# Performance work log

Hardware: AMD Instinct MI355X
Metric: run time of the kernel (lower is better)

The kernel has to match this reference:

```python
import jax, jax.numpy as jnp
import numpy as np

B, S, D, H, V, N_SHARDS, CAP = 4, 512, 512, 8, 32000, 64, 128
HD = D // H


def _layernorm(x, g, b, eps=1e-5):
    mu = x.mean(-1, keepdims=True)
    var = ((x - mu) ** 2).mean(-1, keepdims=True)
    return (x - mu) * jax.lax.rsqrt(var + eps) * g + b


def setup_inputs() -> dict:
    key = jax.random.key(0)
    ks = jax.random.split(key, 16)
    s = 0.02
    return {
        'input_ids': jax.random.randint(ks[0], (B, S), 0, V, dtype=jnp.int32),
        'emb': jax.random.normal(ks[1], (V, D), jnp.float32) * s,
        'Wq': jax.random.normal(ks[2], (D, D), jnp.float32) * s,
        'Wk': jax.random.normal(ks[3], (D, D), jnp.float32) * s,
        'Wv': jax.random.normal(ks[4], (D, D), jnp.float32) * s,
        'Wo': jax.random.normal(ks[5], (D, D), jnp.float32) * s,
        'ln_g': jnp.ones((D,), jnp.float32),
        'ln_b': jnp.zeros((D,), jnp.float32),
        'W_router': jax.random.normal(ks[6], (D, N_SHARDS), jnp.float32),
        'mem_keys': jax.random.normal(ks[7], (N_SHARDS, CAP, D), jnp.float32) * s,
        'mem_values': jax.random.normal(ks[8], (N_SHARDS, CAP, D), jnp.float32) * s,
        'Wg_c': jax.random.normal(ks[9], (D, D), jnp.float32) * s,
        'Wg_m': jax.random.normal(ks[10], (D, D), jnp.float32) * s,
        'bg': jnp.zeros((D,), jnp.float32),
        'Wd': jax.random.normal(ks[11], (D, V), jnp.float32) * s,
        'bd': jnp.zeros((V,), jnp.float32),
        'top_k': 4,
    }


def reference(input_ids, emb, Wq, Wk, Wv, Wo, ln_g, ln_b, W_router,
              mem_keys, mem_values, Wg_c, Wg_m, bg, Wd, bd, top_k):
    # --- encode_context: embedding + causal MHA block (ContextSynthesizer) ---
    x = emb[input_ids]                                   # [B,S,D]
    q = (x @ Wq).reshape(B, S, H, HD)
    k = (x @ Wk).reshape(B, S, H, HD)
    v = (x @ Wv).reshape(B, S, H, HD)
    att = jnp.einsum('bqhd,bkhd->bhqk', q, k) / jnp.sqrt(jnp.float32(HD))
    causal = jnp.tril(jnp.ones((S, S), bool))
    att = jnp.where(causal[None, None], att, jnp.finfo(att.dtype).min)
    att = jax.nn.softmax(att, axis=-1)
    o = jnp.einsum('bhqk,bkhd->bqhd', att, v).reshape(B, S, D) @ Wo
    ctx = _layernorm(x + o, ln_g, ln_b)                  # [B,S,D]

    # --- LSHRouter: hyperplane projection -> shard id per token ---
    routes = jnp.argmax(ctx @ W_router, axis=-1)         # [B,S] int

    # --- MemoryShardStore.query, batched: per-token routed shard top-k read ---
    keys_g = mem_keys[routes]                            # [B,S,CAP,D] irregular gather
    scores = jnp.einsum('bscd,bsd->bsc', keys_g, ctx)    # [B,S,CAP]
    top_v, top_i = jax.lax.top_k(scores, top_k)          # [B,S,k]
    w = jax.nn.softmax(top_v, axis=-1)
    vals = mem_values[routes[:, :, None], top_i]         # [B,S,k,D]
    memory_stream = jnp.einsum('bsk,bskd->bsd', w, vals)

    # --- GatedMemoryFusion ---
    gate = jax.nn.sigmoid(ctx @ Wg_c + memory_stream @ Wg_m + bg)
    fused = gate * ctx + (1.0 - gate) * memory_stream

    # --- decoder; payload bias is zero (store holds no sequence_chunk records) ---
    logits = fused @ Wd + bd                             # [B,S,V]
    return logits
```

## Files before the change

### kernel.cpp

```cpp
#include <hip/hip_runtime.h>

typedef unsigned short u16;
typedef float f32x4 __attribute__((ext_vector_type(4)));
typedef short short8 __attribute__((ext_vector_type(8)));
typedef __bf16 bf16x8 __attribute__((ext_vector_type(8)));

#define B_  4
#define S_  512
#define D_  512
#define H_  8
#define HD_ 64
#define V_  32000
#define NSHARD_ 64
#define CAP_ 128
#define TOK_ (B_ * S_)

__device__ __forceinline__ float bf2f(u16 u) { return __uint_as_float(((unsigned)u) << 16); }
__device__ __forceinline__ u16 f2bf(float f) {
  unsigned u = __float_as_uint(f);
  u += 0x7FFFu + ((u >> 16) & 1u);
  return (u16)(u >> 16);
}

__device__ __forceinline__ f32x4 mfma16(short8 a, short8 b, f32x4 c) {
  return __builtin_amdgcn_mfma_f32_16x16x32_bf16(
      __builtin_bit_cast(bf16x8, a), __builtin_bit_cast(bf16x8, b), c, 0, 0, 0);
}

__device__ __forceinline__ void load_lds16(const void* g, void* l) {
  __builtin_amdgcn_global_load_lds(
      (const __attribute__((address_space(1))) void*)g,
      (__attribute__((address_space(3))) void*)l, 16, 0, 0);
}

template<int NS, bool ACC, int OM, bool CSKIP, bool CKLIM>
__global__ __launch_bounds__(256) void gemm_bt(
    const u16* __restrict__ Ah, const u16* __restrict__ Al, int ldA, long sA1, long sA2,
    const u16* __restrict__ Bh, const u16* __restrict__ Bl, int ldB, long sB1, long sB2,
    void* __restrict__ C0, void* __restrict__ C1, int ldC, long sC1, long sC2,
    int K, int z2n, float alpha)
{
  __shared__ u16 AsH[64 * 64];
  __shared__ u16 BsH[64 * 64];
  __shared__ u16 AsL[(NS == 3) ? 64 * 64 : 8];
  __shared__ u16 BsL[(NS == 3) ? 64 * 64 : 8];

  const int n0 = blockIdx.x * 64;
  const int m0 = blockIdx.y * 64;
  if (CSKIP && n0 > m0 + 63) return;

  const int z = blockIdx.z;
  const int z1 = z / z2n, z2 = z - z1 * z2n;
  const long baseA = (long)z1 * sA1 + (long)z2 * sA2;
  const long baseB = (long)z1 * sB1 + (long)z2 * sB2;
  const long baseC = (long)z1 * sC1 + (long)z2 * sC2;

  const int tid = threadIdx.x;
  const int lane = tid & 63;
  const int w = tid >> 6;
  const int wm = (w >> 1) * 32, wn = (w & 1) * 32;
  const int fr = lane & 15, kg = lane >> 4;

  const int srow = lane >> 3;
  const int schunk = (lane & 7) ^ srow;

  const u16* gAh = Ah + baseA + (long)(m0 + w * 16 + srow) * ldA + schunk * 8;
  const u16* gBh = Bh + baseB + (long)(n0 + w * 16 + srow) * ldB + schunk * 8;
  const u16* gAl = (NS == 3) ? (Al + baseA + (long)(m0 + w * 16 + srow) * ldA + schunk * 8) : nullptr;
  const u16* gBl = (NS == 3) ? (Bl + baseB + (long)(n0 + w * 16 + srow) * ldB + schunk * 8) : nullptr;
  u16* lAh = &AsH[(w * 16) * 64];
  u16* lBh = &BsH[(w * 16) * 64];
  u16* lAl = &AsL[(NS == 3) ? (w * 16) * 64 : 0];
  u16* lBl = &BsL[(NS == 3) ? (w * 16) * 64 : 0];

  const int kmax = CKLIM ? (m0 + 64) : K;

  f32x4 acc[2][2] = {};

  for (int k0 = 0; k0 < kmax; k0 += 64) {
    load_lds16(gAh + k0, lAh);
    load_lds16(gAh + k0 + 8 * ldA, lAh + 8 * 64);
    load_lds16(gBh + k0, lBh);
    load_lds16(gBh + k0 + 8 * ldB, lBh + 8 * 64);
    if (NS == 3) {
      load_lds16(gAl + k0, lAl);
      load_lds16(gAl + k0 + 8 * ldA, lAl + 8 * 64);
      load_lds16(gBl + k0, lBl);
      load_lds16(gBl + k0 + 8 * ldB, lBl + 8 * 64);
    }
    __syncthreads();

    short8 ah[2][2], bh[2][2], al[2][2], bl[2][2];
#pragma unroll
    for (int mi = 0; mi < 2; ++mi) {
      int row = wm + mi * 16 + fr;
#pragma unroll
      for (int ks = 0; ks < 2; ++ks) {
        int idx = row * 64 + ((ks * 32 + kg * 8) ^ ((fr & 7) << 3));
        ah[mi][ks] = *(const short8*)&AsH[idx];
        if (NS == 3) al[mi][ks] = *(const short8*)&AsL[idx];
      }
    }
#pragma unroll
    for (int ni = 0; ni < 2; ++ni) {
      int row = wn + ni * 16 + fr;
#pragma unroll
      for (int ks = 0; ks < 2; ++ks) {
        int idx = row * 64 + ((ks * 32 + kg * 8) ^ ((fr & 7) << 3));
        bh[ni][ks] = *(const short8*)&BsH[idx];
        if (NS == 3) bl[ni][ks] = *(const short8*)&BsL[idx];
      }
    }
#pragma unroll
    for (int ks = 0; ks < 2; ++ks)
#pragma unroll
      for (int mi = 0; mi < 2; ++mi)
#pragma unroll
        for (int ni = 0; ni < 2; ++ni) {
          acc[mi][ni] = mfma16(ah[mi][ks], bh[ni][ks], acc[mi][ni]);
          if (NS == 3) {
            acc[mi][ni] = mfma16(ah[mi][ks], bl[ni][ks], acc[mi][ni]);
            acc[mi][ni] = mfma16(al[mi][ks], bh[ni][ks], acc[mi][ni]);
          }
        }
    __syncthreads();
  }

#pragma unroll
  for (int mi = 0; mi < 2; ++mi)
#pragma unroll
    for (int ni = 0; ni < 2; ++ni) {
      int gnc = n0 + wn + ni * 16 + fr;
#pragma unroll
      for (int r = 0; r < 4; ++r) {
        int gm = m0 + wm + mi * 16 + kg * 4 + r;
        float v = acc[mi][ni][r] * alpha;
        long idx = baseC + (long)gm * ldC + gnc;
        if (OM == 0) {
          float* C = (float*)C0;
          C[idx] = ACC ? (C[idx] + v) : v;
        } else {
          u16 h = f2bf(v);
          ((u16*)C0)[idx] = h;
          ((u16*)C1)[idx] = f2bf(v - bf2f(h));
        }
      }
    }
}

__global__ __launch_bounds__(256) void logits_gemm_k(
    const u16* __restrict__ A, const u16* __restrict__ Bt,
    const float* __restrict__ bias, float* __restrict__ C)
{
  __shared__ u16 As[128 * 64];
  __shared__ u16 Bs[128 * 64];
  const int id = blockIdx.x * 16 + blockIdx.y;
  const int swz = (id & 7) * 500 + (id >> 3);
  const int n0 = (swz / 16) * 128;
  const int m0 = (swz % 16) * 128;
  const int tid = threadIdx.x;
  const int lane = tid & 63;
  const int w = tid >> 6;
  const int wm = (w >> 1) * 64, wn = (w & 1) * 64;
  const int fr = lane & 15, kg = lane >> 4;

  const int srow = lane >> 3;
  const int schunk = (lane & 7) ^ srow;
  const u16* gA = A + (long)(m0 + w * 32 + srow) * D_ + schunk * 8;
  const u16* gB = Bt + (long)(n0 + w * 32 + srow) * D_ + schunk * 8;
  u16* lA = &As[(w * 32) * 64];
  u16* lB = &Bs[(w * 32) * 64];

  f32x4 acc[4][4] = {};

  for (int kt = 0; kt < D_; kt += 64) {
#pragma unroll
    for (int i = 0; i < 4; ++i) {
      load_lds16(gA + (long)i * 8 * D_ + kt, lA + i * 8 * 64);
      load_lds16(gB + (long)i * 8 * D_ + kt, lB + i * 8 * 64);
    }
    __syncthreads();

    short8 af[4][2], bf[4][2];
#pragma unroll
    for (int mi = 0; mi < 4; ++mi) {
      int row = wm + mi * 16 + fr;
#pragma unroll
      for (int ks = 0; ks < 2; ++ks)
        af[mi][ks] = *(const short8*)&As[row * 64 +
                         ((ks * 32 + kg * 8) ^ ((fr & 7) << 3))];
    }
#pragma unroll
    for (int ni = 0; ni < 4; ++ni) {
      int row = wn + ni * 16 + fr;
#pragma unroll
      for (int ks = 0; ks < 2; ++ks)
        bf[ni][ks] = *(const short8*)&Bs[row * 64 +
                         ((ks * 32 + kg * 8) ^ ((fr & 7) << 3))];
    }
#pragma unroll
    for (int ks = 0; ks < 2; ++ks)
#pragma unroll
      for (int mi = 0; mi < 4; ++mi)
#pragma unroll
        for (int ni = 0; ni < 4; ++ni)
          acc[mi][ni] = mfma16(af[mi][ks], bf[ni][ks], acc[mi][ni]);
    __syncthreads();
  }

#pragma unroll
  for (int ni = 0; ni < 4; ++ni) {
    int gnc = n0 + wn + ni * 16 + fr;
    float bv = bias[gnc];
#pragma unroll
    for (int mi = 0; mi < 4; ++mi)
#pragma unroll
      for (int r = 0; r < 4; ++r) {
        int gm = m0 + wm + mi * 16 + kg * 4 + r;
        C[(long)gm * V_ + gnc] = acc[mi][ni][r] + bv;
      }
  }
}

template<bool LO>
__global__ __launch_bounds__(256) void transpose_split_k(
    const float* __restrict__ W, int ldw,
    u16* __restrict__ oh, u16* __restrict__ ol)
{
  __shared__ float t[64][65];
  const int n0 = blockIdx.x * 64;
  const int k0 = blockIdx.y * 64;
  const int tid = threadIdx.x;
  {
    const int kk = tid >> 4;
    const int c4 = (tid & 15) * 4;
#pragma unroll
    for (int i = 0; i < 4; ++i) {
      f32x4 v = *(const f32x4*)(W + (long)(k0 + kk + i * 16) * ldw + n0 + c4);
      t[kk + i * 16][c4] = v[0];
      t[kk + i * 16][c4 + 1] = v[1];
      t[kk + i * 16][c4 + 2] = v[2];
      t[kk + i * 16][c4 + 3] = v[3];
    }
  }
  __syncthreads();
  {
    const int chunk = tid & 7;
    const int nn = tid >> 3;
#pragma unroll
    for (int j = 0; j < 2; ++j) {
      int n = nn + j * 32;
      u16 hbuf[8], lbuf[8];
#pragma unroll
      for (int e = 0; e < 8; ++e) {
        float fv = t[chunk * 8 + e][n];
        u16 h = f2bf(fv);
        hbuf[e] = h;
        if (LO) lbuf[e] = f2bf(fv - bf2f(h));
      }
      long ob = (long)(n0 + n) * 512 + k0 + chunk * 8;
      *(short8*)(oh + ob) = *(short8*)hbuf;
      if (LO) *(short8*)(ol + ob) = *(short8*)lbuf;
    }
  }
}

__global__ __launch_bounds__(256) void v_transpose_k(
    const u16* __restrict__ qh, const u16* __restrict__ ql,
    u16* __restrict__ vTh, u16* __restrict__ vTl)
{
  __shared__ u16 th[64][68];
  __shared__ u16 tl[64][68];
  const int z = blockIdx.y;
  const int b = z >> 3, h = z & 7;
  const int s0 = blockIdx.x * 64;
  const long ibase = ((long)(b * 512 + s0)) * 1536 + 1024 + h * 64;
  const int tid = threadIdx.x;
  {
    const int sr = tid >> 2;
    const int c8 = (tid & 3) * 16;
    const long src = ibase + (long)sr * 1536 + c8;
    *(short8*)&th[sr][c8]     = *(const short8*)(qh + src);
    *(short8*)&th[sr][c8 + 8] = *(const short8*)(qh + src + 8);
    *(short8*)&tl[sr][c8]     = *(const short8*)(ql + src);
    *(short8*)&tl[sr][c8 + 8] = *(const short8*)(ql + src + 8);
  }
  __syncthreads();
  {
    const int dr = tid >> 2;
    const int s8 = (tid & 3) * 16;
    u16 oh[16], ol[16];
#pragma unroll
    for (int j = 0; j < 16; ++j) { oh[j] = th[s8 + j][dr]; ol[j] = tl[s8 + j][dr]; }
    long ob = (long)z * 64 * 512 + (long)dr * 512 + s0 + s8;
    *(short8*)(vTh + ob)     = *(short8*)&oh[0];
    *(short8*)(vTh + ob + 8) = *(short8*)&oh[8];
    *(short8*)(vTl + ob)     = *(short8*)&ol[0];
    *(short8*)(vTl + ob + 8) = *(short8*)&ol[8];
  }
}

__global__ __launch_bounds__(128) void embed_k(const int* __restrict__ ids,
                                               const float* __restrict__ emb,
                                               float* __restrict__ x,
                                               u16* __restrict__ xh,
                                               u16* __restrict__ xl) {
  const int t = blockIdx.x;
  const long id = ids[t];
  const int c = threadIdx.x * 4;
  f32x4 v = *(const f32x4*)(emb + id * (long)D_ + c);
  *(f32x4*)(x + (long)t * D_ + c) = v;
  u16 hh[4], ll[4];
#pragma unroll
  for (int j = 0; j < 4; ++j) {
    u16 h = f2bf(v[j]);
    hh[j] = h;
    ll[j] = f2bf(v[j] - bf2f(h));
  }
  *(unsigned long long*)(xh + (long)t * D_ + c) = *(unsigned long long*)hh;
  *(unsigned long long*)(xl + (long)t * D_ + c) = *(unsigned long long*)ll;
}

__global__ __launch_bounds__(64) void softmax_causal_k(
    const float* __restrict__ att, u16* __restrict__ ph, u16* __restrict__ pl) {
  const int row = blockIdx.x;
  const int i = row & 511;
  const float* p = att + ((long)row << 9);
  const int lane = threadIdx.x;
  float vals[8];
  float m = -3.4e38f;
#pragma unroll
  for (int it = 0; it < 8; ++it) {
    vals[it] = -3.4e38f;
    if (it * 64 <= i) {
      int j = it * 64 + lane;
      float v = (j <= i) ? p[j] : -3.4e38f;
      vals[it] = v;
      m = fmaxf(m, v);
    }
  }
#pragma unroll
  for (int off = 32; off; off >>= 1) m = fmaxf(m, __shfl_xor(m, off));
  float s = 0.f;
#pragma unroll
  for (int it = 0; it < 8; ++it) {
    if (it * 64 <= i) {
      int j = it * 64 + lane;
      float e = (j <= i) ? expf(vals[it] - m) : 0.f;
      vals[it] = e;
      s += e;
    }
  }
#pragma unroll
  for (int off = 32; off; off >>= 1) s += __shfl_xor(s, off);
  float inv = 1.f / s;
#pragma unroll
  for (int it = 0; it < 8; ++it) {
    if (it * 64 <= i) {
      long ob = ((long)row << 9) + it * 64 + lane;
      float e = vals[it] * inv;
      u16 h = f2bf(e);
      ph[ob] = h;
      pl[ob] = f2bf(e - bf2f(h));
    }
  }
}

__global__ __launch_bounds__(256) void resid_ln_k(
    const float* __restrict__ x, const float* __restrict__ proj,
    const float* __restrict__ g, const float* __restrict__ b,
    float* __restrict__ ctxf, u16* __restrict__ ctxh)
{
  const int t = blockIdx.x;
  const int tid = threadIdx.x;
  __shared__ float red[8];
  const float* xr = x + (long)t * D_;
  const float* pr = proj + (long)t * D_;
  float v0 = xr[tid] + pr[tid];
  float v1 = xr[tid + 256] + pr[tid + 256];
  float s = v0 + v1, q = v0 * v0 + v1 * v1;
#pragma unroll
  for (int off = 32; off; off >>= 1) { s += __shfl_xor(s, off); q += __shfl_xor(q, off); }
  const int wave = tid >> 6, lane = tid & 63;
  if (lane == 0) { red[wave] = s; red[4 + wave] = q; }
  __syncthreads();
  s = red[0] + red[1] + red[2] + red[3];
  q = red[4] + red[5] + red[6] + red[7];
  float mu = s * (1.f / 512.f);
  float var = q * (1.f / 512.f) - mu * mu;
  float rs = rsqrtf(var + 1e-5f);
  float o0 = (v0 - mu) * rs * g[tid] + b[tid];
  float o1 = (v1 - mu) * rs * g[tid + 256] + b[tid + 256];
  long base = (long)t * D_;
  ctxf[base + tid] = o0;
  ctxf[base + tid + 256] = o1;
  ctxh[base + tid] = f2bf(o0);
  ctxh[base + tid + 256] = f2bf(o1);
}

__global__ __launch_bounds__(128) void route_mem_k(
    const float* __restrict__ ctxf, const float* __restrict__ Wr,
    const float* __restrict__ keys, const float* __restrict__ valsm,
    float* __restrict__ msf, u16* __restrict__ msh)
{
  const int t = blockIdx.x;
  const int tid = threadIdx.x;
  __shared__ float sctx[D_];
  __shared__ float spart[CAP_];
  __shared__ float sred2[2][64];
  __shared__ int s_route;
  __shared__ int sidx[4];
  __shared__ float sw[4];

  f32x4 cv = ((const f32x4*)(ctxf + (long)t * D_))[tid];
  ((f32x4*)sctx)[tid] = cv;
  __syncthreads();

  {
    const int c = tid & 63, half = tid >> 6;
    float accr = 0.f;
    const float* cp = sctx + half * 256;
    const float* wp = Wr + (long)(half * 256) * NSHARD_ + c;
    for (int d = 0; d < 256; ++d) accr += cp[d] * wp[(long)d * NSHARD_];
    sred2[half][c] = accr;
  }
  __syncthreads();
  if (tid < 64) {
    float v = sred2[0][tid] + sred2[1][tid];
    int idx = tid;
#pragma unroll
    for (int off = 32; off; off >>= 1) {
      float ov = __shfl_xor(v, off);
      int oi = __shfl_xor(idx, off);
      if (ov > v || (ov == v && oi < idx)) { v = ov; idx = oi; }
    }
    if (tid == 0) s_route = idx;
  }
  __syncthreads();
  const int route = s_route;

  {
    const float* krow = keys + ((long)route * CAP_ + tid) * D_;
    float sc = 0.f;
    for (int d0 = 0; d0 < D_; d0 += 4) {
      f32x4 kv = *(const f32x4*)(krow + d0);
      sc += sctx[d0] * kv[0] + sctx[d0 + 1] * kv[1] +
            sctx[d0 + 2] * kv[2] + sctx[d0 + 3] * kv[3];
    }
    spart[tid] = sc;
  }
  __syncthreads();

  for (int rep = 0; rep < 4; ++rep) {
    if (tid < 64) {
      float v1 = spart[tid]; int i1 = tid;
      float v2 = spart[tid + 64]; int i2 = tid + 64;
      float v; int idx;
      if (v2 > v1) { v = v2; idx = i2; } else { v = v1; idx = i1; }
#pragma unroll
      for (int off = 32; off; off >>= 1) {
        float ov = __shfl_xor(v, off);
        int oi = __shfl_xor(idx, off);
        if (ov > v || (ov == v && oi < idx)) { v = ov; idx = oi; }
      }
      if (tid == 0) { sidx[rep] = idx; sw[rep] = v; spart[idx] = -3.4e38f; }
    }
    __syncthreads();
  }

  float w0 = sw[0], w1 = sw[1], w2 = sw[2], w3 = sw[3];
  float mx = fmaxf(fmaxf(w0, w1), fmaxf(w2, w3));
  float e0 = expf(w0 - mx), e1 = expf(w1 - mx), e2 = expf(w2 - mx), e3 = expf(w3 - mx);
  float inv = 1.f / (e0 + e1 + e2 + e3);
  float wk[4] = {e0 * inv, e1 * inv, e2 * inv, e3 * inv};

  float a0 = 0, a1 = 0, a2 = 0, a3 = 0;
#pragma unroll
  for (int k = 0; k < 4; ++k) {
    const float* vr = valsm + ((long)route * CAP_ + sidx[k]) * D_ + tid * 4;
    f32x4 vv = *(const f32x4*)vr;
    float w = wk[k];
    a0 += w * vv[0]; a1 += w * vv[1]; a2 += w * vv[2]; a3 += w * vv[3];
  }
  long ob = (long)t * D_ + tid * 4;
  f32x4 of; of[0] = a0; of[1] = a1; of[2] = a2; of[3] = a3;
  *(f32x4*)(msf + ob) = of;
  u16 oh[4];
  oh[0] = f2bf(a0); oh[1] = f2bf(a1); oh[2] = f2bf(a2); oh[3] = f2bf(a3);
  *(unsigned long long*)(msh + ob) = *(unsigned long long*)oh;
}

__global__ __launch_bounds__(256) void gate_fuse_k(
    const float* __restrict__ g1, const float* __restrict__ bg,
    const float* __restrict__ ctxf, const float* __restrict__ msf,
    u16* __restrict__ fused)
{
  long base = ((long)blockIdx.x * 256 + threadIdx.x) * 4;
  f32x4 gv = *(const f32x4*)(g1 + base);
  f32x4 cv = *(const f32x4*)(ctxf + base);
  f32x4 mv = *(const f32x4*)(msf + base);
  int col = (int)(base & 511);
  u16 o[4];
#pragma unroll
  for (int j = 0; j < 4; ++j) {
    float g = 1.f / (1.f + expf(-(gv[j] + bg[col + j])));
    o[j] = f2bf(g * cv[j] + (1.f - g) * mv[j]);
  }
  *(unsigned long long*)(fused + base) = *(unsigned long long*)o;
}

extern "C" void kernel_launch(void* const* d_in, const int* in_sizes, int n_in,
                              void* d_out, int out_size, void* d_ws, size_t ws_size,
                              hipStream_t stream) {
  const int*   ids  = (const int*)d_in[0];
  const float* emb  = (const float*)d_in[1];
  const float* Wq   = (const float*)d_in[2];
  const float* Wk   = (const float*)d_in[3];
  const float* Wv   = (const float*)d_in[4];
  const float* Wo   = (const float*)d_in[5];
  const float* ln_g = (const float*)d_in[6];
  const float* ln_b = (const float*)d_in[7];
  const float* Wr   = (const float*)d_in[8];
  const float* mk   = (const float*)d_in[9];
  const float* mv   = (const float*)d_in[10];
  const float* Wgc  = (const float*)d_in[11];
  const float* Wgm  = (const float*)d_in[12];
  const float* bg   = (const float*)d_in[13];
  const float* Wd   = (const float*)d_in[14];
  const float* bd   = (const float*)d_in[15];
  float* out = (float*)d_out;

  char* ws = (char*)d_ws;
  size_t off = 0;
  auto alloc = [&](size_t bytes) -> void* {
    void* p = ws + off;
    off += (bytes + 255) & ~(size_t)255;
    return p;
  };
  float* x      = (float*)alloc((size_t)TOK_ * D_ * 4);
  u16*   xh     = (u16*)  alloc((size_t)TOK_ * D_ * 2);
  u16*   xl     = (u16*)  alloc((size_t)TOK_ * D_ * 2);
  u16*   wqkvTh = (u16*)  alloc((size_t)3 * D_ * D_ * 2);
  u16*   wqkvTl = (u16*)  alloc((size_t)3 * D_ * D_ * 2);
  u16*   woTh   = (u16*)  alloc((size_t)D_ * D_ * 2);
  u16*   woTl   = (u16*)  alloc((size_t)D_ * D_ * 2);
  u16*   wgcTh  = (u16*)  alloc((size_t)D_ * D_ * 2);
  u16*   wgmTh  = (u16*)  alloc((size_t)D_ * D_ * 2);
  u16*   wdT    = (u16*)  alloc((size_t)D_ * V_ * 2);
  u16*   qkvh   = (u16*)  alloc((size_t)TOK_ * 3 * D_ * 2);
  u16*   qkvl   = (u16*)  alloc((size_t)TOK_ * 3 * D_ * 2);
  u16*   vTh    = (u16*)  alloc((size_t)B_ * H_ * HD_ * S_ * 2);
  u16*   vTl    = (u16*)  alloc((size_t)B_ * H_ * HD_ * S_ * 2);
  float* att    = (float*)alloc((size_t)B_ * H_ * S_ * S_ * 4);
  u16*   ph     = (u16*)  alloc((size_t)B_ * H_ * S_ * S_ * 2);
  u16*   pl     = (u16*)  alloc((size_t)B_ * H_ * S_ * S_ * 2);
  u16*   oh     = (u16*)  alloc((size_t)TOK_ * D_ * 2);
  u16*   ol     = (u16*)  alloc((size_t)TOK_ * D_ * 2);
  float* proj   = (float*)alloc((size_t)TOK_ * D_ * 4);
  float* ctxf   = (float*)alloc((size_t)TOK_ * D_ * 4);
  u16*   ctxh   = (u16*)  alloc((size_t)TOK_ * D_ * 2);
  float* msf    = (float*)alloc((size_t)TOK_ * D_ * 4);
  u16*   msh    = (u16*)  alloc((size_t)TOK_ * D_ * 2);
  float* g1     = (float*)alloc((size_t)TOK_ * D_ * 4);
  u16*   fused  = (u16*)  alloc((size_t)TOK_ * D_ * 2);

  {
    dim3 g8(D_ / 64, D_ / 64, 1);
    transpose_split_k<true><<<g8, 256, 0, stream>>>(Wq, D_, wqkvTh, wqkvTl);
    transpose_split_k<true><<<g8, 256, 0, stream>>>(Wk, D_, wqkvTh + D_ * D_, wqkvTl + D_ * D_);
    transpose_split_k<true><<<g8, 256, 0, stream>>>(Wv, D_, wqkvTh + 2 * D_ * D_, wqkvTl + 2 * D_ * D_);
    transpose_split_k<true><<<g8, 256, 0, stream>>>(Wo, D_, woTh, woTl);
    transpose_split_k<false><<<g8, 256, 0, stream>>>(Wgc, D_, wgcTh, nullptr);
    transpose_split_k<false><<<g8, 256, 0, stream>>>(Wgm, D_, wgmTh, nullptr);
    dim3 gd(V_ / 64, D_ / 64, 1);
    transpose_split_k<false><<<gd, 256, 0, stream>>>(Wd, V_, wdT, nullptr);
  }

  embed_k<<<TOK_, 128, 0, stream>>>(ids, emb, x, xh, xl);

  {
    dim3 g(1536 / 64, TOK_ / 64, 1);
    gemm_bt<3, false, 1, false, false><<<g, 256, 0, stream>>>(
        xh, xl, D_, 0, 0, wqkvTh, wqkvTl, D_, 0, 0,
        qkvh, qkvl, 1536, 0, 0, D_, 1, 1.f);
  }

  {
    dim3 g(S_ / 64, B_ * H_, 1);
    v_transpose_k<<<g, 256, 0, stream>>>(qkvh, qkvl, vTh, vTl);
  }

  {
    dim3 g(S_ / 64, S_ / 64, B_ * H_);
    gemm_bt<3, false, 0, true, false><<<g, 256, 0, stream>>>(
        qkvh, qkvl, 1536, (long)S_ * 1536, 64,
        qkvh + D_, qkvl + D_, 1536, (long)S_ * 1536, 64,
        att, nullptr, S_, (long)H_ * S_ * S_, (long)S_ * S_,
        HD_, H_, 0.125f);
  }

  softmax_causal_k<<<B_ * H_ * S_, 64, 0, stream>>>(att, ph, pl);

  {
    dim3 g(1, S_ / 64, B_ * H_);
    gemm_bt<3, false, 1, false, true><<<g, 256, 0, stream>>>(
        ph, pl, S_, (long)H_ * S_ * S_, (long)S_ * S_,
        vTh, vTl, S_, (long)H_ * HD_ * S_, (long)HD_ * S_,
        oh, ol, D_, (long)S_ * D_, HD_,
        S_, H_, 1.f);
  }

  {
    dim3 g(D_ / 64, TOK_ / 64, 1);
    gemm_bt<3, false, 0, false, false><<<g, 256, 0, stream>>>(
        oh, ol, D_, 0, 0, woTh, woTl, D_, 0, 0,
        proj, nullptr, D_, 0, 0, D_, 1, 1.f);
  }

  resid_ln_k<<<TOK_, 256, 0, stream>>>(x, proj, ln_g, ln_b, ctxf, ctxh);

  route_mem_k<<<TOK_, 128, 0, stream>>>(ctxf, Wr, mk, mv, msf, msh);

  {
    dim3 g(D_ / 64, TOK_ / 64, 1);
    gemm_bt<1, false, 0, false, false><<<g, 256, 0, stream>>>(
        ctxh, nullptr, D_, 0, 0, wgcTh, nullptr, D_, 0, 0,
        g1, nullptr, D_, 0, 0, D_, 1, 1.f);
    gemm_bt<1, true, 0, false, false><<<g, 256, 0, stream>>>(
        msh, nullptr, D_, 0, 0, wgmTh, nullptr, D_, 0, 0,
        g1, nullptr, D_, 0, 0, D_, 1, 1.f);
  }

  gate_fuse_k<<<(TOK_ * D_) / (256 * 4), 256, 0, stream>>>(g1, bg, ctxf, msf, fused);

  {
    dim3 g(V_ / 128, TOK_ / 128, 1);
    logits_gemm_k<<<g, 256, 0, stream>>>(fused, wdT, bd, out);
  }
}
```

Measured before the change: 345.3 us.

## Rewrite logits GEMM as 256x256 tile, 8-wave, double-buffered ping-pong kernel

Replaces the 128x128 single-buffered logits GEMM with a 256x256 tile kernel run by 512 threads. It double-buffers LDS, interleaves global-to-LDS staging with MFMA quadrants, and orders work with explicit barriers, waitcnt and setprio (a ping-pong schedule). The aim is to hide load latency and raise MFMA utilization on the dominant output GEMM. In exchange it uses 128KB of LDS per block and a hand-tuned waitcnt sequence, which makes correctness fragile, and it launches fewer blocks.

```diff
diff --git a/kernel.cpp b/kernel.cpp
--- a/kernel.cpp
+++ b/kernel.cpp
@@ -148,75 +148,154 @@
     }
 }
 
-__global__ __launch_bounds__(256) void logits_gemm_k(
+__global__ __launch_bounds__(512, 2) void logits_gemm256_k(
     const u16* __restrict__ A, const u16* __restrict__ Bt,
     const float* __restrict__ bias, float* __restrict__ C)
 {
-  __shared__ u16 As[128 * 64];
-  __shared__ u16 Bs[128 * 64];
-  const int id = blockIdx.x * 16 + blockIdx.y;
-  const int swz = (id & 7) * 500 + (id >> 3);
-  const int n0 = (swz / 16) * 128;
-  const int m0 = (swz % 16) * 128;
+  __shared__ u16 As[2][256 * 64];
+  __shared__ u16 Bs[2][256 * 64];
+
+  const int id = blockIdx.x;
+  const int swz = (id & 7) * 125 + (id >> 3);
+  const int n0 = (swz >> 3) * 256;
+  const int m0 = (swz & 7) * 256;
+
   const int tid = threadIdx.x;
   const int lane = tid & 63;
-  const int w = tid >> 6;
-  const int wm = (w >> 1) * 64, wn = (w & 1) * 64;
+  const int wid = tid >> 6;
+  const int wr = wid >> 2, wc = wid & 3;
   const int fr = lane & 15, kg = lane >> 4;
-
   const int srow = lane >> 3;
   const int schunk = (lane & 7) ^ srow;
-  const u16* gA = A + (long)(m0 + w * 32 + srow) * D_ + schunk * 8;
-  const u16* gB = Bt + (long)(n0 + w * 32 + srow) * D_ + schunk * 8;
-  u16* lA = &As[(w * 32) * 64];
-  u16* lB = &Bs[(w * 32) * 64];
-
-  f32x4 acc[4][4] = {};
-
-  for (int kt = 0; kt < D_; kt += 64) {
-#pragma unroll
-    for (int i = 0; i < 4; ++i) {
-      load_lds16(gA + (long)i * 8 * D_ + kt, lA + i * 8 * 64);
-      load_lds16(gB + (long)i * 8 * D_ + kt, lB + i * 8 * 64);
-    }
-    __syncthreads();
-
-    short8 af[4][2], bf[4][2];
-#pragma unroll
-    for (int mi = 0; mi < 4; ++mi) {
-      int row = wm + mi * 16 + fr;
-#pragma unroll
-      for (int ks = 0; ks < 2; ++ks)
-        af[mi][ks] = *(const short8*)&As[row * 64 +
-                         ((ks * 32 + kg * 8) ^ ((fr & 7) << 3))];
-    }
-#pragma unroll
-    for (int ni = 0; ni < 4; ++ni) {
-      int row = wn + ni * 16 + fr;
-#pragma unroll
-      for (int ks = 0; ks < 2; ++ks)
-        bf[ni][ks] = *(const short8*)&Bs[row * 64 +
-                         ((ks * 32 + kg * 8) ^ ((fr & 7) << 3))];
-    }
+
+  f32x4 acc[8][4] = {};
+  short8 pa0[4][2], pa1[4][2], pb0[2][2], pb1[2][2];
+
+  auto stageA = [&](int kt, int h) {
+#pragma unroll
+    for (int j = 0; j < 2; ++j) {
+      int r0 = j * 128 + h * 64 + wid * 8;
+      load_lds16(A + (long)(m0 + r0 + srow) * D_ + kt * 64 + schunk * 8,
+                 &As[kt & 1][r0 * 64]);
+    }
+  };
+  auto stageB = [&](int kt, int h) {
+#pragma unroll
+    for (int j = 0; j < 2; ++j) {
+      int r0 = (j * 2 + (wid >> 2)) * 64 + h * 32 + (wid & 3) * 8;
+      load_lds16(Bt + (long)(n0 + r0 + srow) * D_ + kt * 64 + schunk * 8,
+                 &Bs[kt & 1][r0 * 64]);
+    }
+  };
+  auto readA = [&](short8 (&d)[4][2], int buf, int h) {
+#pragma unroll
+    for (int mi = 0; mi < 4; ++mi)
+#pragma unroll
+      for (int ks = 0; ks < 2; ++ks) {
+        int row = wr * 128 + h * 64 + mi * 16 + fr;
+        d[mi][ks] = *(const short8*)&As[buf][row * 64 +
+                        ((ks * 32 + kg * 8) ^ ((fr & 7) << 3))];
+      }
+  };
+  auto readB = [&](short8 (&d)[2][2], int buf, int h) {
+#pragma unroll
+    for (int ni = 0; ni < 2; ++ni)
+#pragma unroll
+      for (int ks = 0; ks < 2; ++ks) {
+        int row = wc * 64 + h * 32 + ni * 16 + fr;
+        d[ni][ks] = *(const short8*)&Bs[buf][row * 64 +
+                        ((ks * 32 + kg * 8) ^ ((fr & 7) << 3))];
+      }
+  };
+  auto quad = [&](short8 (&a)[4][2], short8 (&b)[2][2], int mb, int nb) {
 #pragma unroll
     for (int ks = 0; ks < 2; ++ks)
 #pragma unroll
       for (int mi = 0; mi < 4; ++mi)
 #pragma unroll
-        for (int ni = 0; ni < 4; ++ni)
-          acc[mi][ni] = mfma16(af[mi][ks], bf[ni][ks], acc[mi][ni]);
-    __syncthreads();
-  }
+        for (int ni = 0; ni < 2; ++ni)
+          acc[mb + mi][nb + ni] = mfma16(a[mi][ks], b[ni][ks], acc[mb + mi][nb + ni]);
+  };
+
+#define SYNC_PRE()                                          \
+  __builtin_amdgcn_sched_barrier(0);                        \
+  __builtin_amdgcn_s_barrier();                             \
+  asm volatile("s_waitcnt lgkmcnt(0)" ::: "memory");        \
+  __builtin_amdgcn_sched_barrier(0);                        \
+  __builtin_amdgcn_s_setprio(1);
+#define SYNC_POST()                                         \
+  __builtin_amdgcn_s_setprio(0);                            \
+  __builtin_amdgcn_sched_barrier(0);                        \
+  __builtin_amdgcn_s_barrier();                             \
+  __builtin_amdgcn_sched_barrier(0);
+
+  stageA(0, 0); stageB(0, 0); stageB(0, 1); stageA(0, 1);
+  stageA(1, 0); stageB(1, 0); stageB(1, 1);
+  __builtin_amdgcn_sched_barrier(0);
+  asm volatile("s_waitcnt vmcnt(6)" ::: "memory");
+  __builtin_amdgcn_s_barrier();
+  __builtin_amdgcn_sched_barrier(0);
+
+  for (int i = 0; i < 4; ++i) {
+    const int t1 = 2 * i + 1, t2 = 2 * i + 2, t3 = 2 * i + 3;
+    const bool st2 = (t2 < 8), st3 = (t3 < 8);
+
+    readA(pa0, 0, 0); readB(pb0, 0, 0);
+    stageA(t1, 1);
+    SYNC_PRE(); quad(pa0, pb0, 0, 0); SYNC_POST();
+
+    readB(pb1, 0, 1);
+    if (st2) stageA(t2, 0);
+    SYNC_PRE(); quad(pa0, pb1, 0, 2); SYNC_POST();
+
+    readA(pa1, 0, 1);
+    if (st2) stageB(t2, 0);
+    SYNC_PRE(); quad(pa1, pb1, 4, 2); SYNC_POST();
+
+    if (st2) stageB(t2, 1);
+    __builtin_amdgcn_sched_barrier(0);
+    if (st2) { asm volatile("s_waitcnt vmcnt(6)" ::: "memory"); }
+    else     { asm volatile("s_waitcnt vmcnt(0)" ::: "memory"); }
+    __builtin_amdgcn_s_barrier();
+    __builtin_amdgcn_sched_barrier(0);
+    __builtin_amdgcn_s_setprio(1);
+    quad(pa1, pb0, 4, 0);
+    SYNC_POST();
+
+    readA(pa0, 1, 0); readB(pb0, 1, 0);
+    if (st2) stageA(t2, 1);
+    SYNC_PRE(); quad(pa0, pb0, 0, 0); SYNC_POST();
+
+    readB(pb1, 1, 1);
+    if (st3) stageA(t3, 0);
+    SYNC_PRE(); quad(pa0, pb1, 0, 2); SYNC_POST();
+
+    readA(pa1, 1, 1);
+    if (st3) stageB(t3, 0);
+    SYNC_PRE(); quad(pa1, pb1, 4, 2); SYNC_POST();
+
+    if (st3) stageB(t3, 1);
+    __builtin_amdgcn_sched_barrier(0);
+    if (st3) { asm volatile("s_waitcnt vmcnt(6)" ::: "memory"); }
+    else     { asm volatile("s_waitcnt vmcnt(0)" ::: "memory"); }
+    __builtin_amdgcn_s_barrier();
+    __builtin_amdgcn_sched_barrier(0);
+    __builtin_amdgcn_s_setprio(1);
+    quad(pa1, pb0, 4, 0);
+    SYNC_POST();
+  }
+#undef SYNC_PRE
+#undef SYNC_POST
 
 #pragma unroll
   for (int ni = 0; ni < 4; ++ni) {
-    int gnc = n0 + wn + ni * 16 + fr;
+    int gnc = n0 + wc * 64 + ni * 16 + fr;
     float bv = bias[gnc];
 #pragma unroll
-    for (int mi = 0; mi < 4; ++mi)
+    for (int mi = 0; mi < 8; ++mi)
 #pragma unroll
       for (int r = 0; r < 4; ++r) {
-        int gm = m0 + wm + mi * 16 + kg * 4 + r;
+        int gm = m0 + wr * 128 + mi * 16 + kg * 4 + r;
         C[(long)gm * V_ + gnc] = acc[mi][ni][r] + bv;
       }
   }
@@ -633,8 +712,5 @@
 
   gate_fuse_k<<<(TOK_ * D_) / (256 * 4), 256, 0, stream>>>(g1, bg, ctxf, msf, fused);
 
-  {
-    dim3 g(V_ / 128, TOK_ / 128, 1);
-    logits_gemm_k<<<g, 256, 0, stream>>>(fused, wdT, bd, out);
-  }
-}
+  logits_gemm256_k<<<1000, 512, 0, stream>>>(fused, wdT, bd, out);
+}
```

Result: no change. 348.5 us (+0.9%).
